# Kernel optimization log

Hardware: AMD Instinct MI355X
Metric: run time of the kernel (lower is better)

Reference implementation:

```python
import jax, jax.numpy as jnp
import numpy as np
import string

N_QUBITS = 16
N_LAYERS = 2
BATCH = 32
DIM = 2 ** N_QUBITS


def _apply_1q(psi, U, q):
    # psi: (B,) + (2,)*n complex; U: (2,2) complex acting on qubit q
    n = psi.ndim - 1
    ax = string.ascii_lowercase[:n]
    out = list(ax)
    out[q] = 'A'
    return jnp.einsum('A' + ax[q] + ',z' + ax + '->z' + ''.join(out), U, psi)


def _apply_2q(psi, G, c, t):
    # G: (2,2,2,2) = (out_c, out_t, in_c, in_t)
    n = psi.ndim - 1
    ax = string.ascii_lowercase[:n]
    out = list(ax)
    out[c] = 'A'
    out[t] = 'B'
    return jnp.einsum('AB' + ax[c] + ax[t] + ',z' + ax + '->z' + ''.join(out), G, psi)


def _rx(th):
    c = jnp.cos(th * 0.5).astype(jnp.complex64)
    s = jnp.sin(th * 0.5).astype(jnp.complex64)
    return jnp.array([[c, -1j * s], [-1j * s, c]])


def _ry(th):
    c = jnp.cos(th * 0.5).astype(jnp.complex64)
    s = jnp.sin(th * 0.5).astype(jnp.complex64)
    return jnp.array([[c, -s], [s, c]])


def _rz(th):
    th_c = th.astype(jnp.complex64)
    z = jnp.zeros((), jnp.complex64)
    return jnp.array([[jnp.exp(-0.5j * th_c), z], [z, jnp.exp(0.5j * th_c)]])


_CNOT = jnp.array([[1, 0, 0, 0],
                   [0, 1, 0, 0],
                   [0, 0, 0, 1],
                   [0, 0, 1, 0]], dtype=jnp.complex64).reshape(2, 2, 2, 2)


def setup_inputs() -> dict:
    key = jax.random.key(0)
    k1, k2, k3 = jax.random.split(key, 3)
    thetas = jax.random.normal(k1, (N_LAYERS, 3, N_QUBITS), dtype=jnp.float32)
    re = jax.random.normal(k2, (BATCH, DIM), dtype=jnp.float32)
    im = jax.random.normal(k3, (BATCH, DIM), dtype=jnp.float32)
    norm = jnp.sqrt(jnp.sum(re * re + im * im, axis=-1, keepdims=True))
    return {"thetas": thetas, "state_re": re / norm, "state_im": im / norm}


def reference(thetas, state_re, state_im):
    B = state_re.shape[0]
    psi = (state_re.astype(jnp.complex64) + 1j * state_im.astype(jnp.complex64))
    psi = psi.reshape((B,) + (2,) * N_QUBITS)
    for l in range(N_LAYERS):
        for q in range(N_QUBITS):
            psi = _apply_1q(psi, _rx(thetas[l, 0, q]), q)
            psi = _apply_1q(psi, _ry(thetas[l, 1, q]), q)
            psi = _apply_1q(psi, _rz(thetas[l, 2, q]), q)
        for q in range(N_QUBITS):
            psi = _apply_2q(psi, _CNOT, q, (q + 1) % N_QUBITS)
    probs = (psi.real ** 2 + psi.imag ** 2).reshape(B, -1)
    return probs
```

## Files before the change

kernel.cpp:

```cpp
#include <hip/hip_runtime.h>


#define NT 256

__device__ __forceinline__ int fperm(int x) {
  int y = x ^ (x >> 1);
  y ^= (x & 1) ? 0xC000 : 0;
  return y & 0xFFFF;
}

__device__ __forceinline__ int finv16(int x) {
  int s = x;
  s ^= s >> 1; s ^= s >> 2; s ^= s >> 4; s ^= s >> 8;
  int b15 = ((s ^ (s >> 15)) & 1) << 15;
  return (s & 0x7FFF) | b15;
}

__device__ __forceinline__ int swz1(int l) { return l ^ ((l >> 4) & 31); }
__device__ __forceinline__ int swz2(int l) { return l ^ ((l >> 5) & 31); }

__device__ __forceinline__ void compute_gates(const float* __restrict__ th, float* gsh) {
  int tid = threadIdx.x;
  if (tid < 32) {
    int l = tid >> 4, q = tid & 15;
    float tx = th[l * 48 + q], ty = th[l * 48 + 16 + q], tz = th[l * 48 + 32 + q];
    float cx, sx, cy, sy, cz, sz;
    sincosf(0.5f * tx, &sx, &cx);
    sincosf(0.5f * ty, &sy, &cy);
    sincosf(0.5f * tz, &sz, &cz);
    float m00r = cy * cx, m00i =  sy * sx;
    float m01r = -sy * cx, m01i = -cy * sx;
    float m10r =  sy * cx, m10i = -cy * sx;
    float m11r =  cy * cx, m11i = -sy * sx;
    float* G = gsh + tid * 8;
    G[0] = cz * m00r + sz * m00i;  G[1] = cz * m00i - sz * m00r;
    G[2] = cz * m01r + sz * m01i;  G[3] = cz * m01i - sz * m01r;
    G[4] = cz * m10r - sz * m10i;  G[5] = cz * m10i + sz * m10r;
    G[6] = cz * m11r - sz * m11i;  G[7] = cz * m11i + sz * m11r;
  }
}

template <int MK, int SK, int N>
__device__ __forceinline__ void greg(float (&ar)[N], float (&ai)[N],
                                     const float* G, int c) {
  const float4* G4 = (const float4*)G;
  float4 r0 = G4[0], r1 = G4[1];
  bool sw = (c != 0);
  float h00r = sw ? r1.z : r0.x, h00i = sw ? r1.w : r0.y;
  float h01r = sw ? r1.x : r0.z, h01i = sw ? r1.y : r0.w;
  float h10r = sw ? r0.z : r1.x, h10i = sw ? r0.w : r1.y;
  float h11r = sw ? r0.x : r1.z, h11i = sw ? r0.y : r1.w;
  constexpr int PV = MK & (-MK);
#pragma unroll
  for (int k = 0; k < N; k++) {
    if (k & PV) continue;
    const int k2 = k ^ MK;
    const int p0 = __builtin_popcount(k & SK) & 1;
    const int ka = p0 ? k2 : k;
    const int kb = p0 ? k : k2;
    float xr = ar[ka], xi = ai[ka], yr = ar[kb], yi = ai[kb];
    ar[ka] = h00r * xr - h00i * xi + h01r * yr - h01i * yi;
    ai[ka] = h00r * xi + h00i * xr + h01r * yi + h01i * yr;
    ar[kb] = h10r * xr - h10i * xi + h11r * yr - h11i * yi;
    ai[kb] = h10r * xi + h10i * xr + h11r * yi + h11i * yr;
  }
}


__device__ __forceinline__ void phaseA_body(int t, int bbase, int wb,
                                            const float* gsh,
                                            float* sre, float* sim,
                                            const float* __restrict__ xre,
                                            const float* __restrict__ xim,
                                            float2* __restrict__ ws) {
  float ar[16], ai[16];
  int base = bbase + (wb << 12);
  const float4* xr4 = (const float4*)(xre + base + (t << 4));
  const float4* xi4 = (const float4*)(xim + base + (t << 4));
#pragma unroll
  for (int q = 0; q < 4; q++) {
    float4 v = xr4[q]; ar[4*q] = v.x; ar[4*q+1] = v.y; ar[4*q+2] = v.z; ar[4*q+3] = v.w;
    float4 w = xi4[q]; ai[4*q] = w.x; ai[4*q+1] = w.y; ai[4*q+2] = w.z; ai[4*q+3] = w.w;
  }
  __syncthreads();
  greg<1, 1>(ar, ai, gsh + 15 * 8, 0);
  greg<2, 2>(ar, ai, gsh + 14 * 8, 0);
  greg<4, 4>(ar, ai, gsh + 13 * 8, 0);
  greg<8, 8>(ar, ai, gsh + 12 * 8, 0);
#pragma unroll
  for (int k = 0; k < 16; k++) { int s = swz1((t << 4) | k); sre[s] = ar[k]; sim[s] = ai[k]; }
  __syncthreads();
#pragma unroll
  for (int k = 0; k < 16; k++) {
    int s = swz1((t & 15) | (k << 4) | ((t >> 4) << 8));
    ar[k] = sre[s]; ai[k] = sim[s];
  }
  greg<1, 1>(ar, ai, gsh + 11 * 8, 0);
  greg<2, 2>(ar, ai, gsh + 10 * 8, 0);
  greg<4, 4>(ar, ai, gsh + 9 * 8, 0);
  greg<8, 8>(ar, ai, gsh + 8 * 8, 0);
#pragma unroll
  for (int k = 0; k < 16; k++) {
    int s = swz1((t & 15) | (k << 4) | ((t >> 4) << 8));
    sre[s] = ar[k]; sim[s] = ai[k];
  }
  __syncthreads();
#pragma unroll
  for (int k = 0; k < 16; k++) {
    int s = swz1(t | (k << 8)); ar[k] = sre[s]; ai[k] = sim[s];
  }
  greg<1, 1>(ar, ai, gsh + 7 * 8, 0);
  greg<2, 2>(ar, ai, gsh + 6 * 8, 0);
  greg<4, 4>(ar, ai, gsh + 5 * 8, 0);
  greg<8, 8>(ar, ai, gsh + 4 * 8, 0);
#pragma unroll
  for (int k = 0; k < 16; k++)
    ws[base + t + (k << 8)] = make_float2(ar[k], ai[k]);
}

__device__ __forceinline__ void phaseB_body(int t, int bbase, int wb,
                                            const float* gsh,
                                            float* sre, float* sim,
                                            float2* __restrict__ ws) {
  float ar[16], ai[16];
#pragma unroll
  for (int k = 0; k < 16; k++) {
    float2 v = ws[bbase + t + (wb << 8) + (k << 12)];
    ar[k] = v.x; ai[k] = v.y;
  }
  int cA = (__popc(t) + __popc(wb)) & 1;
  greg<1, 1>(ar, ai, gsh + 3 * 8, 0);
  greg<2, 2>(ar, ai, gsh + 2 * 8, 0);
  greg<4, 4>(ar, ai, gsh + 1 * 8, 0);
  greg<8, 8>(ar, ai, gsh + 0 * 8, 0);
  greg<12, 7>(ar, ai, gsh + (16 + 0) * 8, cA);
  greg<6, 12>(ar, ai, gsh + (16 + 1) * 8, 0);
  greg<3, 14>(ar, ai, gsh + (16 + 2) * 8, 0);
  __syncthreads();
#pragma unroll
  for (int k = 0; k < 16; k++) {
    int s = swz2(t | (k << 8)); sre[s] = ar[k]; sim[s] = ai[k];
  }
  __syncthreads();
#pragma unroll
  for (int k = 0; k < 16; k++) {
    int s = swz2((k & 3) | (t << 2) | ((k >> 2) << 10));
    ar[k] = sre[s]; ai[k] = sim[s];
  }
  greg<13, 15>(ar, ai, gsh + (16 + 15) * 8, cA);
  greg<3, 14>(ar, ai, gsh + (16 + 14) * 8, cA);
#pragma unroll
  for (int k = 0; k < 16; k++) {
    int s = swz2((k & 3) | (t << 2) | ((k >> 2) << 10));
    sre[s] = ar[k]; sim[s] = ai[k];
  }
  __syncthreads();
#pragma unroll
  for (int k = 0; k < 16; k++) {
    int s = swz2((t & 1) | (k << 1) | ((t >> 1) << 5));
    ar[k] = sre[s]; ai[k] = sim[s];
  }
  {
    int cC = (__popc(t >> 1) + __popc(wb)) & 1;
    greg<3, 14>(ar, ai, gsh + (16 + 13) * 8, cC);
    greg<6, 12>(ar, ai, gsh + (16 + 12) * 8, cC);
    greg<12, 8>(ar, ai, gsh + (16 + 11) * 8, cC);
  }
#pragma unroll
  for (int k = 0; k < 16; k++) {
    int s = swz2((t & 1) | (k << 1) | ((t >> 1) << 5));
    sre[s] = ar[k]; sim[s] = ai[k];
  }
  __syncthreads();
#pragma unroll
  for (int k = 0; k < 16; k++) {
    int s = swz2((t & 15) | (k << 4) | ((t >> 4) << 8));
    ar[k] = sre[s]; ai[k] = sim[s];
  }
  {
    int cD = (__popc(t >> 4) + __popc(wb)) & 1;
    greg<3, 14>(ar, ai, gsh + (16 + 10) * 8, cD);
    greg<6, 12>(ar, ai, gsh + (16 + 9) * 8, cD);
    greg<12, 8>(ar, ai, gsh + (16 + 8) * 8, cD);
  }
#pragma unroll
  for (int k = 0; k < 16; k++) {
    int full = (t & 15) | (k << 4) | (wb << 8) | ((t >> 4) << 12);
    ws[bbase + full] = make_float2(ar[k], ai[k]);
  }
}

__device__ __forceinline__ void phaseC_body(int t, int bbase3, int g3,
                                            const float* gsh,
                                            const float2* __restrict__ ws,
                                            float* __restrict__ out) {
  int jt = t | (g3 << 13);
  float br[32], bi[32];
#pragma unroll
  for (int k = 0; k < 32; k++) {
    int j = jt | (k << 8);
    float2 v = ws[bbase3 + fperm(j)];
    br[k] = v.x; bi[k] = v.y;
  }
  greg<1, 1>(br, bi, gsh + (16 + 7) * 8, 0);
  greg<2, 2>(br, bi, gsh + (16 + 6) * 8, 0);
  greg<4, 4>(br, bi, gsh + (16 + 5) * 8, 0);
  greg<8, 8>(br, bi, gsh + (16 + 4) * 8, 0);
  greg<16, 16>(br, bi, gsh + (16 + 3) * 8, 0);
#pragma unroll
  for (int k = 0; k < 32; k++) {
    int j = jt | (k << 8);
    out[bbase3 + finv16(j)] = br[k] * br[k] + bi[k] * bi[k];
  }
}


__global__ void __launch_bounds__(NT) pass1_k(const float* __restrict__ th,
                                              const float* __restrict__ xre,
                                              const float* __restrict__ xim,
                                              float2* __restrict__ ws) {
  __shared__ float gsh[256];
  __shared__ float sre[4096], sim[4096];
  int t = threadIdx.x;
  int blk = blockIdx.x, batch = blk >> 4, wb = blk & 15;
  compute_gates(th, gsh);
  phaseA_body(t, batch * 65536, wb, gsh, sre, sim, xre, xim, ws);
}

__global__ void __launch_bounds__(NT) pass2_k(const float* __restrict__ th,
                                              float2* __restrict__ ws) {
  __shared__ float gsh[256];
  __shared__ float sre[4096], sim[4096];
  int t = threadIdx.x;
  int blk = blockIdx.x, batch = blk >> 4, wb = blk & 15;
  compute_gates(th, gsh);
  __syncthreads();
  phaseB_body(t, batch * 65536, wb, gsh, sre, sim, ws);
}

__global__ void __launch_bounds__(NT) pass3_k(const float* __restrict__ th,
                                              const float2* __restrict__ ws,
                                              float* __restrict__ out) {
  __shared__ float gsh[256];
  int t = threadIdx.x;
  int blk = blockIdx.x, batch = blk >> 3, g3 = blk & 7;
  compute_gates(th, gsh);
  __syncthreads();
  phaseC_body(t, batch * 65536, g3, gsh, ws, out);
}


__device__ __forceinline__ void signal(unsigned* cnt) {
  __threadfence_block();
  __syncthreads();
  if (threadIdx.x == 0)
    __hip_atomic_fetch_add(cnt, 1u, __ATOMIC_RELEASE, __HIP_MEMORY_SCOPE_AGENT);
}

__device__ __forceinline__ void wait16(unsigned* cnt) {
  if (threadIdx.x == 0) {
    while (__hip_atomic_load(cnt, __ATOMIC_RELAXED, __HIP_MEMORY_SCOPE_AGENT) < 16u)
      __builtin_amdgcn_s_sleep(2);
  }
  __syncthreads();
  __builtin_amdgcn_fence(__ATOMIC_ACQUIRE, "agent");
}

__global__ void __launch_bounds__(NT, 2)
fused_k(const float* __restrict__ th,
        const float* __restrict__ xre, const float* __restrict__ xim,
        float2* __restrict__ ws, float* __restrict__ out,
        unsigned* __restrict__ cnt1, unsigned* __restrict__ cnt2) {
  __shared__ float gsh[256];
  __shared__ float sre[4096], sim[4096];
  int t = threadIdx.x;
  int blk = blockIdx.x;
  int batch = blk >> 4, wb = blk & 15;
  int bbase = batch * 65536;

  compute_gates(th, gsh);
  phaseA_body(t, bbase, wb, gsh, sre, sim, xre, xim, ws);
  signal(&cnt1[batch]);

  wait16(&cnt1[batch]);
  phaseB_body(t, bbase, wb, gsh, sre, sim, ws);
  signal(&cnt2[batch]);

  if (blk >= 256) return;
  int batch3 = blk >> 3, g3 = blk & 7;
  wait16(&cnt2[batch3]);
  phaseC_body(t, batch3 * 65536, g3, gsh, ws, out);
}


extern "C" void kernel_launch(void* const* d_in, const int* in_sizes, int n_in,
                              void* d_out, int out_size, void* d_ws, size_t ws_size,
                              hipStream_t stream) {
  const float* th  = (const float*)d_in[0];
  const float* xre = (const float*)d_in[1];
  const float* xim = (const float*)d_in[2];
  float* out = (float*)d_out;

  float2* amp = (float2*)d_ws;
  unsigned* cnt1 = (unsigned*)((char*)d_ws + (16u << 20));
  unsigned* cnt2 = cnt1 + 32;

  int maxBlk = 0;
  hipError_t qrc = hipOccupancyMaxActiveBlocksPerMultiprocessor(
      &maxBlk, (const void*)fused_k, NT, 0);
  bool use_fused = (qrc == hipSuccess && maxBlk >= 2);

  if (use_fused) {
    hipMemsetAsync((void*)cnt1, 0, 64 * sizeof(unsigned), stream);
    fused_k<<<512, NT, 0, stream>>>(th, xre, xim, amp, out, cnt1, cnt2);
  } else {
    pass1_k<<<512, NT, 0, stream>>>(th, xre, xim, amp);
    pass2_k<<<512, NT, 0, stream>>>(th, amp);
    pass3_k<<<256, NT, 0, stream>>>(th, amp, out);
  }
}
```

Baseline: 103.8 us.

## Map batches to XCDs and skip agent-scope acquire fence when producers share XCD

Remaps block indices so that all blocks of one batch are likely dispatched to the same XCD, assuming round-robin block-to-XCD assignment. Each signaling block records its hardware XCC id in a per-batch bitmask. Waiters skip the agent-scope acquire fence when all producers ran on one XCD, avoiding an L2 invalidate. The risk is correctness: skipping the fence relies on same-XCD L2 coherence and on non-temporal or cached visibility assumptions.

Result: no change. 105.6 us (+1.8%).

```diff
diff --git a/kernel.cpp b/kernel.cpp
--- a/kernel.cpp
+++ b/kernel.cpp
@@ -250,45 +250,61 @@
 }
 
 
-__device__ __forceinline__ void signal(unsigned* cnt) {
+__device__ __forceinline__ void signal(unsigned* cnt, unsigned* msk, unsigned xcd) {
   __threadfence_block();
   __syncthreads();
-  if (threadIdx.x == 0)
+  if (threadIdx.x == 0) {
+    __hip_atomic_fetch_or(msk, 1u << (xcd & 31), __ATOMIC_RELAXED, __HIP_MEMORY_SCOPE_AGENT);
     __hip_atomic_fetch_add(cnt, 1u, __ATOMIC_RELEASE, __HIP_MEMORY_SCOPE_AGENT);
-}
-
-__device__ __forceinline__ void wait16(unsigned* cnt) {
+  }
+}
+
+__device__ __forceinline__ void wait16(unsigned* cnt, unsigned* msk, unsigned* sflag) {
   if (threadIdx.x == 0) {
     while (__hip_atomic_load(cnt, __ATOMIC_RELAXED, __HIP_MEMORY_SCOPE_AGENT) < 16u)
       __builtin_amdgcn_s_sleep(2);
-  }
-  __syncthreads();
-  __builtin_amdgcn_fence(__ATOMIC_ACQUIRE, "agent");
+    unsigned m = __hip_atomic_load(msk, __ATOMIC_RELAXED, __HIP_MEMORY_SCOPE_AGENT);
+    *sflag = ((m & (m - 1u)) == 0u) ? 1u : 0u;
+  }
+  __syncthreads();
+  if (*sflag == 0u)
+    __builtin_amdgcn_fence(__ATOMIC_ACQUIRE, "agent");
 }
 
 __global__ void __launch_bounds__(NT, 2)
 fused_k(const float* __restrict__ th,
         const float* __restrict__ xre, const float* __restrict__ xim,
         float2* __restrict__ ws, float* __restrict__ out,
-        unsigned* __restrict__ cnt1, unsigned* __restrict__ cnt2) {
+        unsigned* __restrict__ sync) {
   __shared__ float gsh[256];
   __shared__ float sre[4096], sim[4096];
+  __shared__ unsigned sflag;
   int t = threadIdx.x;
   int blk = blockIdx.x;
-  int batch = blk >> 4, wb = blk & 15;
+
+  int xcd_hint = blk & 7, w = blk >> 3;
+  int batch = xcd_hint * 4 + (w & 3), wb = w >> 2;
   int bbase = batch * 65536;
+
+  unsigned xcc;
+  asm volatile("s_getreg_b32 %0, hwreg(HW_REG_XCC_ID)" : "=s"(xcc));
+
+  unsigned* cnt1 = sync;
+  unsigned* msk1 = sync + 32;
+  unsigned* cnt2 = sync + 64;
+  unsigned* msk2 = sync + 96;
 
   compute_gates(th, gsh);
   phaseA_body(t, bbase, wb, gsh, sre, sim, xre, xim, ws);
-  signal(&cnt1[batch]);
-
-  wait16(&cnt1[batch]);
+  signal(&cnt1[batch], &msk1[batch], xcc);
+
+  wait16(&cnt1[batch], &msk1[batch], &sflag);
   phaseB_body(t, bbase, wb, gsh, sre, sim, ws);
-  signal(&cnt2[batch]);
+  signal(&cnt2[batch], &msk2[batch], xcc);
 
   if (blk >= 256) return;
-  int batch3 = blk >> 3, g3 = blk & 7;
-  wait16(&cnt2[batch3]);
+  int batch3 = (blk & 7) * 4 + ((blk >> 3) & 3), g3 = blk >> 5;
+  wait16(&cnt2[batch3], &msk2[batch3], &sflag);
   phaseC_body(t, batch3 * 65536, g3, gsh, ws, out);
 }
 
@@ -302,8 +318,7 @@
   float* out = (float*)d_out;
 
   float2* amp = (float2*)d_ws;
-  unsigned* cnt1 = (unsigned*)((char*)d_ws + (16u << 20));
-  unsigned* cnt2 = cnt1 + 32;
+  unsigned* sync = (unsigned*)((char*)d_ws + (16u << 20));
 
   int maxBlk = 0;
   hipError_t qrc = hipOccupancyMaxActiveBlocksPerMultiprocessor(
@@ -311,8 +326,8 @@
   bool use_fused = (qrc == hipSuccess && maxBlk >= 2);
 
   if (use_fused) {
-    hipMemsetAsync((void*)cnt1, 0, 64 * sizeof(unsigned), stream);
-    fused_k<<<512, NT, 0, stream>>>(th, xre, xim, amp, out, cnt1, cnt2);
+    hipMemsetAsync((void*)sync, 0, 128 * sizeof(unsigned), stream);
+    fused_k<<<512, NT, 0, stream>>>(th, xre, xim, amp, out, sync);
   } else {
     pass1_k<<<512, NT, 0, stream>>>(th, xre, xim, amp);
     pass2_k<<<512, NT, 0, stream>>>(th, amp);
```
